# Optimization experiments

Hardware: AMD Instinct MI355X
Metric: run time of the kernel (lower is better)

Reference implementation:

```python
import jax, jax.numpy as jnp
import numpy as np

DIM = 1024
RANK = 16


def setup_inputs() -> dict:
    key = jax.random.key(0)
    ks = jax.random.split(key, 9)
    s = 0.02
    return {
        "x": jax.random.normal(ks[0], (2, 4096, DIM), dtype=jnp.float32),
        "W_qkv": jax.random.normal(ks[1], (3 * DIM, DIM), dtype=jnp.float32) * s,
        "b_qkv": jax.random.normal(ks[2], (3 * DIM,), dtype=jnp.float32) * s,
        "A_q": jax.random.normal(ks[3], (RANK, DIM), dtype=jnp.float32) * s,
        "B_q": jax.random.normal(ks[4], (DIM, RANK), dtype=jnp.float32) * s,
        "A_k": jax.random.normal(ks[5], (RANK, DIM), dtype=jnp.float32) * s,
        "B_k": jax.random.normal(ks[6], (DIM, RANK), dtype=jnp.float32) * s,
        "A_v": jax.random.normal(ks[7], (RANK, DIM), dtype=jnp.float32) * s,
        "B_v": jax.random.normal(ks[8], (DIM, RANK), dtype=jnp.float32) * s,
        "alpha": jnp.float32(0.5),
    }


def reference(x, W_qkv, b_qkv, A_q, B_q, A_k, B_k, A_v, B_v, alpha):
    # base fused QKV projection: [B, S, 3*dim]
    qkv = jnp.einsum("bsd,od->bso", x, W_qkv) + b_qkv
    # low-rank adapters: x @ A.T @ B.T, rank=16
    lora_q = jnp.einsum("bsr,dr->bsd", jnp.einsum("bsd,rd->bsr", x, A_q), B_q)
    lora_k = jnp.einsum("bsr,dr->bsd", jnp.einsum("bsd,rd->bsr", x, A_k), B_k)
    lora_v = jnp.einsum("bsr,dr->bsd", jnp.einsum("bsd,rd->bsr", x, A_v), B_v)
    # scaled add into q/k/v slices (concat order matches torch slice layout)
    delta = jnp.concatenate([lora_q, lora_k, lora_v], axis=-1)
    return qkv + alpha * delta
```

## Files before the change

### kernel.cpp

```cpp
#include <hip/hip_runtime.h>
#include <stdint.h>

#define DIM    1024
#define RANK   16
#define M_TOT  8192
#define N_TOT  3072
#define K_TOT  1024

#define BM 256
#define BN 128
#define BK 64
#define NT (K_TOT / BK)

typedef __attribute__((ext_vector_type(8))) short  s8v;
typedef __attribute__((ext_vector_type(4))) float  f4v;

__device__ __forceinline__ unsigned short f2bf(float f) {
    union { float f; unsigned int u; } v; v.f = f;
    unsigned int u = v.u;
    u += 0x7FFFu + ((u >> 16) & 1u);
    return (unsigned short)(u >> 16);
}

__device__ __forceinline__ void gload_lds16(const unsigned short* g,
                                            unsigned short* l) {
    __builtin_amdgcn_global_load_lds(
        (const __attribute__((address_space(1))) void*)g,
        (__attribute__((address_space(3))) void*)l,
        16, 0, 0);
}

__global__ __launch_bounds__(256)
void prep(const float4* __restrict__ x, ushort4* __restrict__ xb,
          const float* __restrict__ W,
          const float* __restrict__ Aq, const float* __restrict__ Bq,
          const float* __restrict__ Ak, const float* __restrict__ Bk,
          const float* __restrict__ Av, const float* __restrict__ Bv,
          const float* __restrict__ alpha_p,
          unsigned short* __restrict__ Wb) {
    const int tid = threadIdx.x;
    if (blockIdx.x < 2048) {
        int i = blockIdx.x * 256 + tid;
        #pragma unroll
        for (int k = 0; k < 4; ++k) {
            float4 v = x[i];
            ushort4 o;
            o.x = f2bf(v.x); o.y = f2bf(v.y); o.z = f2bf(v.z); o.w = f2bf(v.w);
            xb[i] = o;
            i += 2048 * 256;
        }
    } else {
        const int bid2 = blockIdx.x - 2048;
        const int sel  = bid2 >> 6;
        const int rb   = bid2 & 63;
        const float* Am = (sel == 0) ? Aq : (sel == 1) ? Ak : Av;
        const float* Bm = (sel == 0) ? Bq : (sel == 1) ? Bk : Bv;

        __shared__ float sb[16][RANK];
        {
            const int row = rb * 16 + (tid >> 4);
            sb[tid >> 4][tid & 15] = alpha_p[0] * Bm[row * RANK + (tid & 15)];
        }
        __syncthreads();

        float4 a4[RANK];
        #pragma unroll
        for (int r = 0; r < RANK; ++r)
            a4[r] = ((const float4*)(Am + r * DIM))[tid];

        #pragma unroll
        for (int row = 0; row < 16; ++row) {
            const int o = sel * 1024 + rb * 16 + row;
            float4 w = ((const float4*)(W + (size_t)o * DIM))[tid];
            #pragma unroll
            for (int r = 0; r < RANK; ++r) {
                const float s = sb[row][r];
                w.x += s * a4[r].x; w.y += s * a4[r].y;
                w.z += s * a4[r].z; w.w += s * a4[r].w;
            }
            ushort4 ov;
            ov.x = f2bf(w.x); ov.y = f2bf(w.y); ov.z = f2bf(w.z); ov.w = f2bf(w.w);
            ((ushort4*)(Wb + (size_t)o * DIM))[tid] = ov;
        }
    }
}

__global__ __launch_bounds__(512, 2)
void gemm_bt(const unsigned short* __restrict__ Xb,
             const unsigned short* __restrict__ Wb,
             const float* __restrict__ bias,
             float* __restrict__ out) {
    __shared__ __align__(16) unsigned short As[3][BM * BK];
    __shared__ __align__(16) unsigned short Bs[3][BN * BK];

    const int tid  = threadIdx.x;
    const int wave = tid >> 6;
    const int lane = tid & 63;
    const int l15  = lane & 15;
    const int lq   = lane >> 4;
    const int wr   = wave >> 1;
    const int wc   = wave & 1;

    const int bid   = blockIdx.x;
    const int xcd   = bid & 7;
    const int s     = bid >> 3;
    const int chunk = s >> 5;
    const int t5    = s & 31;
    const int bm    = xcd * 4 + (t5 >> 3);
    const int bn    = chunk * 8 + (t5 & 7);

    const unsigned short* aptr[4];
    const unsigned short* bptr[2];
    int aoff[4], boff[2];
    #pragma unroll
    for (int u = 0; u < 4; ++u) {
        const int c   = wave * 4 + u;
        const int row = ((c >> 1) << 4) + l15;
        const int col = ((c & 1) << 5) + (lq << 3);
        aptr[u] = Xb + (size_t)(bm * BM + row) * K_TOT + col;
        aoff[u] = c * 512;
    }
    #pragma unroll
    for (int u = 0; u < 2; ++u) {
        const int c   = wave * 2 + u;
        const int row = ((c >> 1) << 4) + l15;
        const int col = ((c & 1) << 5) + (lq << 3);
        bptr[u] = Wb + (size_t)(bn * BN + row) * K_TOT + col;
        boff[u] = c * 512;
    }

    #pragma unroll
    for (int t = 0; t < 2; ++t) {
        #pragma unroll
        for (int u = 0; u < 4; ++u) gload_lds16(aptr[u] + t * BK, &As[t][aoff[u]]);
        #pragma unroll
        for (int u = 0; u < 2; ++u) gload_lds16(bptr[u] + t * BK, &Bs[t][boff[u]]);
    }
    asm volatile("s_waitcnt vmcnt(6)" ::: "memory");
    __builtin_amdgcn_sched_barrier(0);
    __builtin_amdgcn_s_barrier();
    __builtin_amdgcn_sched_barrier(0);

    f4v acc[4][4] = {};

    #pragma unroll
    for (int q = 0; q < NT; ++q) {
        const int r    = q % 3;
        const int r2   = (q + 2) % 3;
        const int kg   = (q + 2) * BK;
        const bool iss = (q + 2) < NT;

        const s8v* Avp = (const s8v*)As[r];
        const s8v* Bvp = (const s8v*)Bs[r];

        #pragma unroll
        for (int t = 0; t < 2; ++t) {
            s8v af[4], bf[4];
            #pragma unroll
            for (int i = 0; i < 4; ++i) {
                af[i] = Avp[((wr * 4 + i) * 2 + t) * 64 + lane];
                bf[i] = Bvp[((wc * 4 + i) * 2 + t) * 64 + lane];
            }
            if (iss) {
                if (t == 0) {
                    gload_lds16(aptr[0] + kg, &As[r2][aoff[0]]);
                    gload_lds16(aptr[1] + kg, &As[r2][aoff[1]]);
                    gload_lds16(bptr[0] + kg, &Bs[r2][boff[0]]);
                } else {
                    gload_lds16(aptr[2] + kg, &As[r2][aoff[2]]);
                    gload_lds16(aptr[3] + kg, &As[r2][aoff[3]]);
                    gload_lds16(bptr[1] + kg, &Bs[r2][boff[1]]);
                }
            }
            __builtin_amdgcn_s_barrier();
            asm volatile("s_waitcnt lgkmcnt(0)" ::: "memory");
            __builtin_amdgcn_sched_barrier(0);
            __builtin_amdgcn_s_setprio(1);
            #pragma unroll
            for (int i = 0; i < 4; ++i)
                #pragma unroll
                for (int j = 0; j < 4; ++j)
                    acc[i][j] = __builtin_amdgcn_mfma_f32_16x16x32_bf16(
                        af[i], bf[j], acc[i][j], 0, 0, 0);
            __builtin_amdgcn_s_setprio(0);

            if (t == 0) {
                __builtin_amdgcn_s_barrier();
            } else {
                if (q < NT - 2)
                    asm volatile("s_waitcnt vmcnt(6)" ::: "memory");
                else if (q == NT - 2)
                    asm volatile("s_waitcnt vmcnt(0)" ::: "memory");
                if (q < NT - 1) {
                    __builtin_amdgcn_sched_barrier(0);
                    __builtin_amdgcn_s_barrier();
                    __builtin_amdgcn_sched_barrier(0);
                }
            }
        }
    }

    const int col_base = bn * BN + wc * 64;
    const int row_base = bm * BM + wr * 64 + lq * 4;
    #pragma unroll
    for (int j = 0; j < 4; ++j) {
        const int col = col_base + j * 16 + l15;
        const float bv = bias[col];
        #pragma unroll
        for (int i = 0; i < 4; ++i) {
            const int row = row_base + i * 16;
            #pragma unroll
            for (int r = 0; r < 4; ++r)
                out[(size_t)(row + r) * N_TOT + col] = acc[i][j][r] + bv;
        }
    }
}

extern "C" void kernel_launch(void* const* d_in, const int* in_sizes, int n_in,
                              void* d_out, int out_size, void* d_ws, size_t ws_size,
                              hipStream_t stream) {
    const float* x     = (const float*)d_in[0];
    const float* W     = (const float*)d_in[1];
    const float* b     = (const float*)d_in[2];
    const float* Aq    = (const float*)d_in[3];
    const float* Bq    = (const float*)d_in[4];
    const float* Ak    = (const float*)d_in[5];
    const float* Bk    = (const float*)d_in[6];
    const float* Av    = (const float*)d_in[7];
    const float* Bv    = (const float*)d_in[8];
    const float* alpha = (const float*)d_in[9];
    float* out = (float*)d_out;

    unsigned short* xb = (unsigned short*)d_ws;
    unsigned short* Wb = (unsigned short*)((char*)d_ws + (size_t)M_TOT * K_TOT * 2);

    prep<<<2048 + 192, 256, 0, stream>>>((const float4*)x, (ushort4*)xb,
                                         W, Aq, Bq, Ak, Bk, Av, Bv, alpha, Wb);

    gemm_bt<<<(M_TOT / BM) * (N_TOT / BN), 512, 0, stream>>>(xb, Wb, b, out);
}
```

Before: 245.6 us.

## Replace direct-to-LDS triple buffering with register-staged single-buffer GEMM loop

Drops the async global_load_lds triple-buffered pipeline and its hand-placed barriers, waitcnts and setprio. Instead each k-step loads the next tile into registers, writes it to one shared LDS buffer between two __syncthreads, and then runs the MFMAs. This cuts LDS use per block and raises the launch-bounds occupancy hint, and the tile-to-block mapping is changed to sweep all 24 column tiles per row group. The trade is that the loop is now fully serialized at each barrier, and staging through registers adds VGPR pressure and extra LDS store instructions.

```diff
diff --git a/kernel.cpp b/kernel.cpp
--- a/kernel.cpp
+++ b/kernel.cpp
@@ -20,14 +20,6 @@
     unsigned int u = v.u;
     u += 0x7FFFu + ((u >> 16) & 1u);
     return (unsigned short)(u >> 16);
-}
-
-__device__ __forceinline__ void gload_lds16(const unsigned short* g,
-                                            unsigned short* l) {
-    __builtin_amdgcn_global_load_lds(
-        (const __attribute__((address_space(1))) void*)g,
-        (__attribute__((address_space(3))) void*)l,
-        16, 0, 0);
 }
 
 __global__ __launch_bounds__(256)
@@ -85,13 +77,12 @@
     }
 }
 
-__global__ __launch_bounds__(512, 2)
+__global__ __launch_bounds__(512, 6)
 void gemm_bt(const unsigned short* __restrict__ Xb,
              const unsigned short* __restrict__ Wb,
              const float* __restrict__ bias,
              float* __restrict__ out) {
-    __shared__ __align__(16) unsigned short As[3][BM * BK];
-    __shared__ __align__(16) unsigned short Bs[3][BN * BK];
+    __shared__ __align__(16) unsigned short S[48 * 512];
 
     const int tid  = threadIdx.x;
     const int wave = tid >> 6;
@@ -101,58 +92,47 @@
     const int wr   = wave >> 1;
     const int wc   = wave & 1;
 
-    const int bid   = blockIdx.x;
-    const int xcd   = bid & 7;
-    const int s     = bid >> 3;
-    const int chunk = s >> 5;
-    const int t5    = s & 31;
-    const int bm    = xcd * 4 + (t5 >> 3);
-    const int bn    = chunk * 8 + (t5 & 7);
+    const int bid = blockIdx.x;
+    const int xcd = bid & 7;
+    const int s   = bid >> 3;
+    const int bm  = xcd * 4 + s / 24;
+    const int bn  = s % 24;
 
-    const unsigned short* aptr[4];
-    const unsigned short* bptr[2];
-    int aoff[4], boff[2];
+    const unsigned short* gp[6];
+    unsigned short* lp[6];
     #pragma unroll
-    for (int u = 0; u < 4; ++u) {
-        const int c   = wave * 4 + u;
-        const int row = ((c >> 1) << 4) + l15;
+    for (int u = 0; u < 6; ++u) {
+        const int c = wave * 6 + u;
         const int col = ((c & 1) << 5) + (lq << 3);
-        aptr[u] = Xb + (size_t)(bm * BM + row) * K_TOT + col;
-        aoff[u] = c * 512;
-    }
-    #pragma unroll
-    for (int u = 0; u < 2; ++u) {
-        const int c   = wave * 2 + u;
-        const int row = ((c >> 1) << 4) + l15;
-        const int col = ((c & 1) << 5) + (lq << 3);
-        bptr[u] = Wb + (size_t)(bn * BN + row) * K_TOT + col;
-        boff[u] = c * 512;
+        if (c < 32) {
+            const int row = ((c >> 1) << 4) + l15;
+            gp[u] = Xb + (size_t)(bm * BM + row) * K_TOT + col;
+        } else {
+            const int row = (((c - 32) >> 1) << 4) + l15;
+            gp[u] = Wb + (size_t)(bn * BN + row) * K_TOT + col;
+        }
+        lp[u] = &S[c * 512 + lane * 8];
     }
 
+    s8v reg[6];
     #pragma unroll
-    for (int t = 0; t < 2; ++t) {
-        #pragma unroll
-        for (int u = 0; u < 4; ++u) gload_lds16(aptr[u] + t * BK, &As[t][aoff[u]]);
-        #pragma unroll
-        for (int u = 0; u < 2; ++u) gload_lds16(bptr[u] + t * BK, &Bs[t][boff[u]]);
-    }
-    asm volatile("s_waitcnt vmcnt(6)" ::: "memory");
-    __builtin_amdgcn_sched_barrier(0);
-    __builtin_amdgcn_s_barrier();
-    __builtin_amdgcn_sched_barrier(0);
+    for (int u = 0; u < 6; ++u) reg[u] = *(const s8v*)(gp[u]);
 
     f4v acc[4][4] = {};
 
-    #pragma unroll
-    for (int q = 0; q < NT; ++q) {
-        const int r    = q % 3;
-        const int r2   = (q + 2) % 3;
-        const int kg   = (q + 2) * BK;
-        const bool iss = (q + 2) < NT;
+    for (int kk = 0; kk < K_TOT; kk += BK) {
+        __syncthreads();
+        #pragma unroll
+        for (int u = 0; u < 6; ++u)
+            *(s8v*)(lp[u]) = reg[u];
+        __syncthreads();
 
-        const s8v* Avp = (const s8v*)As[r];
-        const s8v* Bvp = (const s8v*)Bs[r];
+        const int kn = (kk + BK < K_TOT) ? (kk + BK) : 0;
+        #pragma unroll
+        for (int u = 0; u < 6; ++u) reg[u] = *(const s8v*)(gp[u] + kn);
 
+        const s8v* Avp = (const s8v*)S;
+        const s8v* Bvp = (const s8v*)S + 2048;
         #pragma unroll
         for (int t = 0; t < 2; ++t) {
             s8v af[4], bf[4];
@@ -161,42 +141,12 @@
                 af[i] = Avp[((wr * 4 + i) * 2 + t) * 64 + lane];
                 bf[i] = Bvp[((wc * 4 + i) * 2 + t) * 64 + lane];
             }
-            if (iss) {
-                if (t == 0) {
-                    gload_lds16(aptr[0] + kg, &As[r2][aoff[0]]);
-                    gload_lds16(aptr[1] + kg, &As[r2][aoff[1]]);
-                    gload_lds16(bptr[0] + kg, &Bs[r2][boff[0]]);
-                } else {
-                    gload_lds16(aptr[2] + kg, &As[r2][aoff[2]]);
-                    gload_lds16(aptr[3] + kg, &As[r2][aoff[3]]);
-                    gload_lds16(bptr[1] + kg, &Bs[r2][boff[1]]);
-                }
-            }
-            __builtin_amdgcn_s_barrier();
-            asm volatile("s_waitcnt lgkmcnt(0)" ::: "memory");
-            __builtin_amdgcn_sched_barrier(0);
-            __builtin_amdgcn_s_setprio(1);
             #pragma unroll
             for (int i = 0; i < 4; ++i)
                 #pragma unroll
                 for (int j = 0; j < 4; ++j)
                     acc[i][j] = __builtin_amdgcn_mfma_f32_16x16x32_bf16(
                         af[i], bf[j], acc[i][j], 0, 0, 0);
-            __builtin_amdgcn_s_setprio(0);
-
-            if (t == 0) {
-                __builtin_amdgcn_s_barrier();
-            } else {
-                if (q < NT - 2)
-                    asm volatile("s_waitcnt vmcnt(6)" ::: "memory");
-                else if (q == NT - 2)
-                    asm volatile("s_waitcnt vmcnt(0)" ::: "memory");
-                if (q < NT - 1) {
-                    __builtin_amdgcn_sched_barrier(0);
-                    __builtin_amdgcn_s_barrier();
-                    __builtin_amdgcn_sched_barrier(0);
-                }
-            }
         }
     }
 
```

New measurement: 507.5 us. +106.6%, slower.
